# Performance work log

Measured on AMD Instinct MI355X. Metric: run time of the kernel, lower is better.

Reference implementation:

```python
import jax, jax.numpy as jnp
import numpy as np

IN_F = 4096
OUT_F = 4096
ORDER = 8
N_ROWS = 8192


def setup_inputs() -> dict:
    key = jax.random.key(0)
    ks = jax.random.split(key, 10)
    maxf = max(IN_F, OUT_F)
    minf = min(IN_F, OUT_F)
    return {
        "x": jax.random.normal(ks[0], (N_ROWS, IN_F), jnp.float32),
        "v_mean": jax.random.normal(ks[1], (ORDER, maxf), jnp.float32),
        "v_logvar": jax.random.normal(ks[2], (ORDER, maxf), jnp.float32) - 5.0,
        "d_mean": jax.random.normal(ks[3], (minf,), jnp.float32),
        "d_logvar": jax.random.normal(ks[4], (minf,), jnp.float32) - 5.0,
        "bias_mean": jax.random.normal(ks[5], (OUT_F,), jnp.float32) * 0.01,
        "bias_logvar": jax.random.normal(ks[6], (OUT_F,), jnp.float32) * 0.01 - 5.0,
        "eps_v": jax.random.normal(ks[7], (ORDER, maxf), jnp.float32),
        "eps_d": jax.random.normal(ks[8], (minf,), jnp.float32),
        "eps_b": jax.random.normal(ks[9], (OUT_F,), jnp.float32),
    }


def _householder_chain(v_normed, dtype):
    # Product H_0 @ H_1 @ ... @ H_{k-1}, H_i = I - 2 v_i v_i^T, via rank-1 updates:
    # P @ H_i = P - 2 (P v_i) v_i^T  -- mathematically identical to the dense
    # eye-expand + mm chain in the torch module, O(order*F^2) instead of O(order*F^3).
    maxf = v_normed.shape[1]

    def step(P, vi):
        Pv = P @ vi                      # [F]
        return P - 2.0 * Pv[:, None] * vi[None, :], None

    u, _ = jax.lax.scan(step, jnp.eye(maxf, dtype=dtype), v_normed)
    return u


def reference(x, v_mean, v_logvar, d_mean, d_logvar, bias_mean, bias_logvar,
              eps_v, eps_d, eps_b):
    # Reparameterized samples
    v = v_mean + jnp.exp(0.5 * v_logvar) * eps_v        # [order, maxF]
    d = d_mean + jnp.exp(0.5 * d_logvar) * eps_d        # [minF]
    bias = bias_mean + jnp.exp(0.5 * bias_logvar) * eps_b  # [out]

    vn = v / jnp.linalg.norm(v, axis=1, keepdims=True)
    u = _householder_chain(vn, x.dtype)                 # [maxF, maxF] orthogonal

    if OUT_F <= IN_F:
        # W = u @ eye(in,out) @ diag(d) == first OUT_F cols of u, scaled by d
        W = u[:, :OUT_F] * d[None, :]                   # [in, out]
    else:
        # W = diag(d) @ eye(in,out) @ u == first IN_F rows of u, scaled by d
        W = d[:, None] * u[:IN_F, :]                    # [in, out]

    return x @ W + bias[None, :]
```

## Files before the change

### kernel.cpp

```cpp
#include <hip/hip_runtime.h>

#define ORDER 8
#define FDIM 4096
#define NROWS 8192
#define THREADS 256
#define RPB 4
#define F4T 4
#define F4DIM (FDIM/4)

__global__ __launch_bounds__(THREADS) void obd_prep(
    const float* __restrict__ v_mean, const float* __restrict__ v_logvar,
    const float* __restrict__ eps_v,
    const float* __restrict__ d_mean, const float* __restrict__ d_logvar,
    const float* __restrict__ eps_d,
    const float* __restrict__ b_mean, const float* __restrict__ b_logvar,
    const float* __restrict__ eps_b,
    float* __restrict__ vn, float* __restrict__ dsc, float* __restrict__ bias)
{
    const int b = blockIdx.x;
    const int t = threadIdx.x;
    __shared__ float red[THREADS / 64];

    if (b < ORDER) {
        const float4* vm = (const float4*)(v_mean   + (size_t)b * FDIM);
        const float4* vl = (const float4*)(v_logvar + (size_t)b * FDIM);
        const float4* ev = (const float4*)(eps_v    + (size_t)b * FDIM);
        float4 val[F4T];
        float ss = 0.f;
        #pragma unroll
        for (int k = 0; k < F4T; ++k) {
            const int idx = t + k * THREADS;
            float4 m = vm[idx], l = vl[idx], e = ev[idx];
            float4 v;
            v.x = fmaf(expf(0.5f * l.x), e.x, m.x);
            v.y = fmaf(expf(0.5f * l.y), e.y, m.y);
            v.z = fmaf(expf(0.5f * l.z), e.z, m.z);
            v.w = fmaf(expf(0.5f * l.w), e.w, m.w);
            val[k] = v;
            ss += v.x * v.x + v.y * v.y + v.z * v.z + v.w * v.w;
        }
        #pragma unroll
        for (int off = 32; off; off >>= 1) ss += __shfl_down(ss, off);
        const int wave = t >> 6, lane = t & 63;
        if (lane == 0) red[wave] = ss;
        __syncthreads();
        const float tot = red[0] + red[1] + red[2] + red[3];
        const float inv = 1.0f / sqrtf(tot);
        float4* vno = (float4*)(vn + (size_t)b * FDIM);
        #pragma unroll
        for (int k = 0; k < F4T; ++k) {
            const int idx = t + k * THREADS;
            float4 v = val[k];
            v.x *= inv; v.y *= inv; v.z *= inv; v.w *= inv;
            vno[idx] = v;
        }
    } else if (b == ORDER) {
        #pragma unroll
        for (int k = 0; k < 16; ++k) {
            const int idx = t + k * THREADS;
            dsc[idx] = fmaf(expf(0.5f * d_logvar[idx]), eps_d[idx], d_mean[idx]);
        }
    } else {
        #pragma unroll
        for (int k = 0; k < 16; ++k) {
            const int idx = t + k * THREADS;
            bias[idx] = fmaf(expf(0.5f * b_logvar[idx]), eps_b[idx], b_mean[idx]);
        }
    }
}

__global__ __launch_bounds__(THREADS) void obd_apply(
    const float* __restrict__ x, const float* __restrict__ vn,
    const float* __restrict__ dsc, const float* __restrict__ bias,
    float* __restrict__ out)
{
    const int t = threadIdx.x;
    const size_t row0 = (size_t)blockIdx.x * RPB;
    const float4* xv = (const float4*)x;
    float4* ov = (float4*)out;

    float4 r[RPB][F4T];
    #pragma unroll
    for (int rr = 0; rr < RPB; ++rr) {
        const size_t base = (row0 + rr) * F4DIM;
        #pragma unroll
        for (int k = 0; k < F4T; ++k)
            r[rr][k] = xv[base + t + k * THREADS];
    }

    __shared__ float4 red[ORDER][THREADS / 64];
    const int wave = t >> 6, lane = t & 63;

    #pragma unroll
    for (int i = 0; i < ORDER; ++i) {
        const float4* vrow = (const float4*)(vn + (size_t)i * FDIM);
        float4 vc[F4T];
        float p[RPB] = {0.f, 0.f, 0.f, 0.f};
        #pragma unroll
        for (int k = 0; k < F4T; ++k) {
            vc[k] = vrow[t + k * THREADS];
            #pragma unroll
            for (int rr = 0; rr < RPB; ++rr) {
                p[rr] = fmaf(r[rr][k].x, vc[k].x, p[rr]);
                p[rr] = fmaf(r[rr][k].y, vc[k].y, p[rr]);
                p[rr] = fmaf(r[rr][k].z, vc[k].z, p[rr]);
                p[rr] = fmaf(r[rr][k].w, vc[k].w, p[rr]);
            }
        }
        #pragma unroll
        for (int off = 32; off; off >>= 1) {
            #pragma unroll
            for (int rr = 0; rr < RPB; ++rr)
                p[rr] += __shfl_down(p[rr], off);
        }
        if (lane == 0) red[i][wave] = make_float4(p[0], p[1], p[2], p[3]);
        __syncthreads();
        const float4 a0 = red[i][0], a1 = red[i][1], a2 = red[i][2], a3 = red[i][3];
        const float dot[RPB] = { a0.x + a1.x + a2.x + a3.x,
                                 a0.y + a1.y + a2.y + a3.y,
                                 a0.z + a1.z + a2.z + a3.z,
                                 a0.w + a1.w + a2.w + a3.w };
        #pragma unroll
        for (int rr = 0; rr < RPB; ++rr) {
            const float c = -2.0f * dot[rr];
            #pragma unroll
            for (int k = 0; k < F4T; ++k) {
                r[rr][k].x = fmaf(c, vc[k].x, r[rr][k].x);
                r[rr][k].y = fmaf(c, vc[k].y, r[rr][k].y);
                r[rr][k].z = fmaf(c, vc[k].z, r[rr][k].z);
                r[rr][k].w = fmaf(c, vc[k].w, r[rr][k].w);
            }
        }
    }

    #pragma unroll
    for (int k = 0; k < F4T; ++k) {
        const int idx = t + k * THREADS;
        const float4 dd = ((const float4*)dsc)[idx];
        const float4 bb = ((const float4*)bias)[idx];
        #pragma unroll
        for (int rr = 0; rr < RPB; ++rr) {
            float4 o;
            o.x = fmaf(r[rr][k].x, dd.x, bb.x);
            o.y = fmaf(r[rr][k].y, dd.y, bb.y);
            o.z = fmaf(r[rr][k].z, dd.z, bb.z);
            o.w = fmaf(r[rr][k].w, dd.w, bb.w);
            ov[(row0 + rr) * F4DIM + idx] = o;
        }
    }
}

extern "C" void kernel_launch(void* const* d_in, const int* in_sizes, int n_in,
                              void* d_out, int out_size, void* d_ws, size_t ws_size,
                              hipStream_t stream) {
    const float* x        = (const float*)d_in[0];
    const float* v_mean   = (const float*)d_in[1];
    const float* v_logvar = (const float*)d_in[2];
    const float* d_mean   = (const float*)d_in[3];
    const float* d_logvar = (const float*)d_in[4];
    const float* b_mean   = (const float*)d_in[5];
    const float* b_logvar = (const float*)d_in[6];
    const float* eps_v    = (const float*)d_in[7];
    const float* eps_d    = (const float*)d_in[8];
    const float* eps_b    = (const float*)d_in[9];

    float* ws   = (float*)d_ws;
    float* vn   = ws;
    float* dsc  = ws + ORDER * FDIM;
    float* bias = ws + ORDER * FDIM + FDIM;

    obd_prep<<<ORDER + 2, THREADS, 0, stream>>>(
        v_mean, v_logvar, eps_v, d_mean, d_logvar, eps_d,
        b_mean, b_logvar, eps_b, vn, dsc, bias);
    obd_apply<<<NROWS / RPB, THREADS, 0, stream>>>(
        x, vn, dsc, bias, (float*)d_out);
}
```

Before: 66.32 us.

## Replace sequential Householder reflections with compact WY representation

Applies the Householder chain through a compact WY form, (I - V^T T V) with a small triangular T. A new single-block kernel builds T from the Gram matrix of the normalized vectors. The apply kernel now computes all eight dot products per row in one pass with a single block-wide reduction and barrier, instead of eight serialized reduce/sync rounds. The cost is an extra kernel launch, a second read of V, and more registers for the per-row dot and coefficient arrays.

```diff
diff --git a/kernel.cpp b/kernel.cpp
--- a/kernel.cpp
+++ b/kernel.cpp
@@ -7,6 +7,7 @@
 #define RPB 4
 #define F4T 4
 #define F4DIM (FDIM/4)
+#define NPAIR 36
 
 __global__ __launch_bounds__(THREADS) void obd_prep(
     const float* __restrict__ v_mean, const float* __restrict__ v_logvar,
@@ -44,8 +45,7 @@
         const int wave = t >> 6, lane = t & 63;
         if (lane == 0) red[wave] = ss;
         __syncthreads();
-        const float tot = red[0] + red[1] + red[2] + red[3];
-        const float inv = 1.0f / sqrtf(tot);
+        const float inv = 1.0f / sqrtf(red[0] + red[1] + red[2] + red[3]);
         float4* vno = (float4*)(vn + (size_t)b * FDIM);
         #pragma unroll
         for (int k = 0; k < F4T; ++k) {
@@ -69,15 +69,92 @@
     }
 }
 
-__global__ __launch_bounds__(THREADS) void obd_apply(
-    const float* __restrict__ x, const float* __restrict__ vn,
-    const float* __restrict__ dsc, const float* __restrict__ bias,
-    float* __restrict__ out)
+__global__ __launch_bounds__(THREADS) void obd_gramT(
+    const float* __restrict__ vn, float* __restrict__ Tm)
 {
     const int t = threadIdx.x;
+    const int wave = t >> 6, lane = t & 63;
+    const float4* Vv = (const float4*)vn;
+
+    float acc[ORDER][ORDER];
+    #pragma unroll
+    for (int i = 0; i < ORDER; ++i)
+        #pragma unroll
+        for (int j = i; j < ORDER; ++j) acc[i][j] = 0.f;
+
+    #pragma unroll
+    for (int k = 0; k < F4T; ++k) {
+        const int idx = t + k * THREADS;
+        float4 vc[ORDER];
+        #pragma unroll
+        for (int i = 0; i < ORDER; ++i) vc[i] = Vv[i * F4DIM + idx];
+        #pragma unroll
+        for (int i = 0; i < ORDER; ++i)
+            #pragma unroll
+            for (int j = i; j < ORDER; ++j) {
+                acc[i][j] = fmaf(vc[i].x, vc[j].x, acc[i][j]);
+                acc[i][j] = fmaf(vc[i].y, vc[j].y, acc[i][j]);
+                acc[i][j] = fmaf(vc[i].z, vc[j].z, acc[i][j]);
+                acc[i][j] = fmaf(vc[i].w, vc[j].w, acc[i][j]);
+            }
+    }
+    #pragma unroll
+    for (int off = 32; off; off >>= 1)
+        #pragma unroll
+        for (int i = 0; i < ORDER; ++i)
+            #pragma unroll
+            for (int j = i; j < ORDER; ++j)
+                acc[i][j] += __shfl_down(acc[i][j], off);
+
+    __shared__ float red[THREADS / 64][NPAIR];
+    if (lane == 0) {
+        int p = 0;
+        #pragma unroll
+        for (int i = 0; i < ORDER; ++i)
+            #pragma unroll
+            for (int j = i; j < ORDER; ++j) red[wave][p++] = acc[i][j];
+    }
+    __syncthreads();
+    if (t == 0) {
+        float G[ORDER][ORDER];
+        int p = 0;
+        for (int i = 0; i < ORDER; ++i)
+            for (int j = i; j < ORDER; ++j) {
+                G[i][j] = red[0][p] + red[1][p] + red[2][p] + red[3][p];
+                ++p;
+            }
+        float T[ORDER][ORDER];
+        for (int i = 0; i < ORDER; ++i)
+            for (int j = 0; j < ORDER; ++j) T[i][j] = 0.f;
+        T[0][0] = 2.f;
+        for (int j = 1; j < ORDER; ++j) {
+            for (int i = 0; i < j; ++i) {
+                float s = 0.f;
+                for (int m = i; m < j; ++m) s += T[i][m] * G[m][j];
+                T[i][j] = -2.f * s;
+            }
+            T[j][j] = 2.f;
+        }
+        for (int i = 0; i < ORDER; ++i)
+            for (int j = 0; j < ORDER; ++j) Tm[i * ORDER + j] = T[i][j];
+    }
+}
+
+__global__ __launch_bounds__(THREADS, 4) void obd_wy(
+    const float* __restrict__ x, const float* __restrict__ vn,
+    const float* __restrict__ Tm, const float* __restrict__ dsc,
+    const float* __restrict__ bias, float* __restrict__ out)
+{
+    const int t = threadIdx.x;
+    const int wave = t >> 6, lane = t & 63;
     const size_t row0 = (size_t)blockIdx.x * RPB;
     const float4* xv = (const float4*)x;
+    const float4* Vv = (const float4*)vn;
     float4* ov = (float4*)out;
+
+    __shared__ float Ts[64];
+    __shared__ float red[THREADS / 64][RPB * ORDER];
+    if (t < 64) Ts[t] = Tm[t];
 
     float4 r[RPB][F4T];
     #pragma unroll
@@ -88,56 +165,78 @@
             r[rr][k] = xv[base + t + k * THREADS];
     }
 
-    __shared__ float4 red[ORDER][THREADS / 64];
-    const int wave = t >> 6, lane = t & 63;
-
-    #pragma unroll
-    for (int i = 0; i < ORDER; ++i) {
-        const float4* vrow = (const float4*)(vn + (size_t)i * FDIM);
-        float4 vc[F4T];
-        float p[RPB] = {0.f, 0.f, 0.f, 0.f};
-        #pragma unroll
-        for (int k = 0; k < F4T; ++k) {
-            vc[k] = vrow[t + k * THREADS];
-            #pragma unroll
-            for (int rr = 0; rr < RPB; ++rr) {
-                p[rr] = fmaf(r[rr][k].x, vc[k].x, p[rr]);
-                p[rr] = fmaf(r[rr][k].y, vc[k].y, p[rr]);
-                p[rr] = fmaf(r[rr][k].z, vc[k].z, p[rr]);
-                p[rr] = fmaf(r[rr][k].w, vc[k].w, p[rr]);
-            }
-        }
-        #pragma unroll
-        for (int off = 32; off; off >>= 1) {
-            #pragma unroll
-            for (int rr = 0; rr < RPB; ++rr)
-                p[rr] += __shfl_down(p[rr], off);
-        }
-        if (lane == 0) red[i][wave] = make_float4(p[0], p[1], p[2], p[3]);
-        __syncthreads();
-        const float4 a0 = red[i][0], a1 = red[i][1], a2 = red[i][2], a3 = red[i][3];
-        const float dot[RPB] = { a0.x + a1.x + a2.x + a3.x,
-                                 a0.y + a1.y + a2.y + a3.y,
-                                 a0.z + a1.z + a2.z + a3.z,
-                                 a0.w + a1.w + a2.w + a3.w };
-        #pragma unroll
-        for (int rr = 0; rr < RPB; ++rr) {
-            const float c = -2.0f * dot[rr];
-            #pragma unroll
-            for (int k = 0; k < F4T; ++k) {
-                r[rr][k].x = fmaf(c, vc[k].x, r[rr][k].x);
-                r[rr][k].y = fmaf(c, vc[k].y, r[rr][k].y);
-                r[rr][k].z = fmaf(c, vc[k].z, r[rr][k].z);
-                r[rr][k].w = fmaf(c, vc[k].w, r[rr][k].w);
-            }
-        }
-    }
+    float p[RPB][ORDER];
+    #pragma unroll
+    for (int rr = 0; rr < RPB; ++rr)
+        #pragma unroll
+        for (int i = 0; i < ORDER; ++i) p[rr][i] = 0.f;
 
     #pragma unroll
     for (int k = 0; k < F4T; ++k) {
         const int idx = t + k * THREADS;
-        const float4 dd = ((const float4*)dsc)[idx];
-        const float4 bb = ((const float4*)bias)[idx];
+        #pragma unroll
+        for (int i = 0; i < ORDER; ++i) {
+            const float4 vc = Vv[i * F4DIM + idx];
+            #pragma unroll
+            for (int rr = 0; rr < RPB; ++rr) {
+                p[rr][i] = fmaf(r[rr][k].x, vc.x, p[rr][i]);
+                p[rr][i] = fmaf(r[rr][k].y, vc.y, p[rr][i]);
+                p[rr][i] = fmaf(r[rr][k].z, vc.z, p[rr][i]);
+                p[rr][i] = fmaf(r[rr][k].w, vc.w, p[rr][i]);
+            }
+        }
+    }
+    #pragma unroll
+    for (int off = 32; off; off >>= 1)
+        #pragma unroll
+        for (int rr = 0; rr < RPB; ++rr)
+            #pragma unroll
+            for (int i = 0; i < ORDER; ++i)
+                p[rr][i] += __shfl_down(p[rr][i], off);
+    if (lane == 0) {
+        #pragma unroll
+        for (int rr = 0; rr < RPB; ++rr)
+            #pragma unroll
+            for (int i = 0; i < ORDER; ++i)
+                red[wave][rr * ORDER + i] = p[rr][i];
+    }
+    __syncthreads();
+
+    float mq[RPB][ORDER];
+    #pragma unroll
+    for (int rr = 0; rr < RPB; ++rr) {
+        float dot[ORDER];
+        #pragma unroll
+        for (int i = 0; i < ORDER; ++i)
+            dot[i] = red[0][rr * ORDER + i] + red[1][rr * ORDER + i]
+                   + red[2][rr * ORDER + i] + red[3][rr * ORDER + i];
+        #pragma unroll
+        for (int j = 0; j < ORDER; ++j) {
+            float s = 0.f;
+            #pragma unroll
+            for (int i = 0; i <= j; ++i) s = fmaf(dot[i], Ts[i * ORDER + j], s);
+            mq[rr][j] = -s;
+        }
+    }
+
+    const float4* dv = (const float4*)dsc;
+    const float4* bv = (const float4*)bias;
+    #pragma unroll
+    for (int k = 0; k < F4T; ++k) {
+        const int idx = t + k * THREADS;
+        #pragma unroll
+        for (int i = 0; i < ORDER; ++i) {
+            const float4 vc = Vv[i * F4DIM + idx];
+            #pragma unroll
+            for (int rr = 0; rr < RPB; ++rr) {
+                r[rr][k].x = fmaf(mq[rr][i], vc.x, r[rr][k].x);
+                r[rr][k].y = fmaf(mq[rr][i], vc.y, r[rr][k].y);
+                r[rr][k].z = fmaf(mq[rr][i], vc.z, r[rr][k].z);
+                r[rr][k].w = fmaf(mq[rr][i], vc.w, r[rr][k].w);
+            }
+        }
+        const float4 dd = dv[idx];
+        const float4 bb = bv[idx];
         #pragma unroll
         for (int rr = 0; rr < RPB; ++rr) {
             float4 o;
@@ -168,10 +267,12 @@
     float* vn   = ws;
     float* dsc  = ws + ORDER * FDIM;
     float* bias = ws + ORDER * FDIM + FDIM;
+    float* Tm   = ws + ORDER * FDIM + 2 * FDIM;
 
     obd_prep<<<ORDER + 2, THREADS, 0, stream>>>(
         v_mean, v_logvar, eps_v, d_mean, d_logvar, eps_d,
         b_mean, b_logvar, eps_b, vn, dsc, bias);
-    obd_apply<<<NROWS / RPB, THREADS, 0, stream>>>(
-        x, vn, dsc, bias, (float*)d_out);
-}
+    obd_gramT<<<1, THREADS, 0, stream>>>(vn, Tm);
+    obd_wy<<<NROWS / RPB, THREADS, 0, stream>>>(
+        x, vn, Tm, dsc, bias, (float*)d_out);
+}
```

Result: slower. 174.8 us (+163.6%).
